# Kernel optimization log

Measured on AMD Instinct MI355X. Metric: run time of the kernel, lower is better.

The kernel has to match this reference:

```python
import jax, jax.numpy as jnp
import numpy as np
import math

B, L, H = 2, 2048, 2048
NH, HD, RD = 16, 128, 64
QR, KVR = 768, 512


def rotate_half(x):
    d = x.shape[-1]
    x1, x2 = x[..., : d // 2], x[..., d // 2 :]
    return jnp.concatenate([-x2, x1], axis=-1)


def apply_rope(x):
    # x: [B, L, H, D] or [B, L, D]
    d = x.shape[-1]
    seq_len = x.shape[1]
    inv_freq = 1.0 / (10000.0 ** (jnp.arange(0, d, 2, dtype=x.dtype) / d))
    pos = jnp.arange(seq_len, dtype=x.dtype)
    freqs = jnp.outer(pos, inv_freq)  # [L, d/2]
    cos = jnp.concatenate([jnp.cos(freqs), jnp.cos(freqs)], axis=-1)  # [L, d]
    sin = jnp.concatenate([jnp.sin(freqs), jnp.sin(freqs)], axis=-1)
    if x.ndim == 4:
        cos, sin = cos[None, :, None, :], sin[None, :, None, :]
    else:
        cos, sin = cos[None, :, :], sin[None, :, :]
    return x * cos + rotate_half(x) * sin


def setup_inputs() -> dict:
    key = jax.random.key(0)
    ks = jax.random.split(key, 9)
    sc = lambda fan_in: 1.0 / math.sqrt(fan_in)
    return {
        "x": jax.random.normal(ks[0], (B, L, H), jnp.float32),
        "wq_down": jax.random.normal(ks[1], (H, QR), jnp.float32) * sc(H),
        "wq_up": jax.random.normal(ks[2], (QR, NH * HD), jnp.float32) * sc(QR),
        "wq_rope": jax.random.normal(ks[3], (QR, NH * RD), jnp.float32) * sc(QR),
        "wkv_down": jax.random.normal(ks[4], (H, KVR), jnp.float32) * sc(H),
        "wk_up": jax.random.normal(ks[5], (KVR, NH * HD), jnp.float32) * sc(KVR),
        "wv_up": jax.random.normal(ks[6], (KVR, NH * HD), jnp.float32) * sc(KVR),
        "wk_rope": jax.random.normal(ks[7], (H, RD), jnp.float32) * sc(H),
        "wo": jax.random.normal(ks[8], (NH * HD, H), jnp.float32) * sc(NH * HD),
    }


def reference(x, wq_down, wq_up, wq_rope, wkv_down, wk_up, wv_up, wk_rope, wo):
    b, l, _ = x.shape
    # Q low-rank path
    q_latent = x @ wq_down                              # [B,L,QR]
    q_content = (q_latent @ wq_up).reshape(b, l, NH, HD)
    q_rope = (q_latent @ wq_rope).reshape(b, l, NH, RD)
    q_rope = apply_rope(q_rope)
    # KV joint low-rank path
    kv_latent = x @ wkv_down                            # [B,L,KVR]
    k_content = (kv_latent @ wk_up).reshape(b, l, NH, HD)
    v = (kv_latent @ wv_up).reshape(b, l, NH, HD)
    # decoupled RoPE key (shared across heads)
    k_rope = apply_rope(x @ wk_rope)                    # [B,L,RD]
    k_rope = jnp.broadcast_to(k_rope[:, :, None, :], (b, l, NH, RD))
    q = jnp.concatenate([q_content, q_rope], axis=-1)   # [B,L,NH,HD+RD]
    k = jnp.concatenate([k_content, k_rope], axis=-1)
    scale = 1.0 / math.sqrt(HD + RD)
    scores = jnp.einsum("bqhd,bkhd->bhqk", q, k) * scale
    causal_mask = jnp.triu(jnp.ones((l, l), dtype=bool), k=1)
    scores = jnp.where(causal_mask[None, None], -jnp.inf, scores)
    attn = jax.nn.softmax(scores, axis=-1)
    out = jnp.einsum("bhqk,bkhd->bqhd", attn, v).reshape(b, l, NH * HD)
    return out @ wo
```

## Files before the change

### kernel.cpp

```cpp
#include <hip/hip_runtime.h>

typedef unsigned short u16;
typedef unsigned int u32;
typedef unsigned long long u64;
typedef __bf16 bf16x8 __attribute__((ext_vector_type(8)));
typedef float f32x4 __attribute__((ext_vector_type(4)));
typedef float f32x16 __attribute__((ext_vector_type(16)));
typedef u32 u32x4 __attribute__((ext_vector_type(4)));

#define DEV static __device__ __forceinline__

constexpr int B_ = 2, L_ = 2048, H_ = 2048;
constexpr int NH_ = 16, HD_ = 128, RD_ = 64;
constexpr int QR_ = 768, KVR_ = 512;
constexpr int BL_ = B_ * L_;
constexpr int QKD_ = HD_ + RD_;
constexpr int QKS_ = NH_ * QKD_;
constexpr int NHHD_ = NH_ * HD_;
constexpr int ROWS_ = B_ * NH_ * L_;
constexpr float SCALE2 = 0.07216878364870322f * 1.4426950408889634f;

DEV u16 f2bf(float f) {
    __bf16 h = (__bf16)f;
    return __builtin_bit_cast(u16, h);
}
DEV float bf2f(u16 h) {
    u32 u = ((u32)h) << 16;
    return __builtin_bit_cast(float, u);
}
DEV u32 pk2(float lo, float hi) { return (u32)f2bf(lo) | ((u32)f2bf(hi) << 16); }
DEV bf16x8 ld8(const u16* p) { return __builtin_bit_cast(bf16x8, *(const u32x4*)p); }
DEV f32x4 mfma16(bf16x8 a, bf16x8 b, f32x4 c) {
    return __builtin_amdgcn_mfma_f32_16x16x32_bf16(a, b, c, 0, 0, 0);
}
DEV f32x16 mfma32(bf16x8 a, bf16x8 b, f32x16 c) {
    return __builtin_amdgcn_mfma_f32_32x32x16_bf16(a, b, c, 0, 0, 0);
}
DEV void gload16(const void* g, void* l) {
    __builtin_amdgcn_global_load_lds((const __attribute__((address_space(1))) void*)g,
                                     (__attribute__((address_space(3))) void*)l, 16, 0, 0);
}

__global__ __launch_bounds__(256) void cast_bf16_kernel(const float* __restrict__ src,
                                                        u16* __restrict__ dst, int n4) {
    int i = blockIdx.x * 256 + threadIdx.x;
    if (i >= n4) return;
    float4 v = ((const float4*)src)[i];
    u64 pk = (u64)f2bf(v.x) | ((u64)f2bf(v.y) << 16) | ((u64)f2bf(v.z) << 32) | ((u64)f2bf(v.w) << 48);
    ((u64*)dst)[i] = pk;
}

__global__ __launch_bounds__(256) void cast_transpose(const float* __restrict__ src, u16* __restrict__ dst,
                                                      int K, int N, int dstN) {
    __shared__ float tile[32][33];
    int n0 = blockIdx.x * 32, k0 = blockIdx.y * 32;
    int tx = threadIdx.x & 31, ty = threadIdx.x >> 5;
#pragma unroll
    for (int i = 0; i < 4; ++i) {
        int kk = ty + i * 8;
        int n = n0 + tx;
        tile[kk][tx] = (n < N) ? src[(size_t)(k0 + kk) * N + n] : 0.f;
    }
    __syncthreads();
#pragma unroll
    for (int i = 0; i < 4; ++i) {
        int nn = ty + i * 8;
        dst[(size_t)(n0 + nn) * K + k0 + tx] = f2bf(tile[tx][nn]);
    }
}

__global__ __launch_bounds__(256) void build_rope_tab(float2* __restrict__ tab) {
    int idx = blockIdx.x * 256 + threadIdx.x;
    int pos = idx >> 5, i = idx & 31;
    float freq = exp2f((float)i * (-13.287712379549449f / 32.f));
    float ang = (float)pos * freq;
    tab[idx] = make_float2(cosf(ang), sinf(ang));
}

template <int EPI>
__global__ __launch_bounds__(256, 2) void gemm_bt(const u16* __restrict__ A, int lda,
                                                  const u16* __restrict__ Bt,
                                                  void* __restrict__ Cv, void* __restrict__ Cv2,
                                                  int ldc, int K, const float2* __restrict__ tab) {
    __shared__ u16 As[128 * 64];
    __shared__ u16 Bs[128 * 64];
    const int tid = threadIdx.x;
    const int l = tid & 63, w = tid >> 6;
    const int l15 = l & 15, g = l >> 4;
    const int wr = w >> 1, wc = w & 1;
    const int bm = blockIdx.y * 128, bn = blockIdx.x * 128;

    const f32x4 zero = {0.f, 0.f, 0.f, 0.f};
    f32x4 acc[4][4];
#pragma unroll
    for (int m = 0; m < 4; ++m)
#pragma unroll
        for (int n = 0; n < 4; ++n) acc[m][n] = zero;

    int aoff[4], boff[4];
#pragma unroll
    for (int j = 0; j < 4; ++j) {
        int chunk = j * 256 + tid;
        int row = chunk >> 3, gr = chunk & 7;
        aoff[j] = row * lda + gr * 8;
        boff[j] = row * K + gr * 8;
    }
    const u16* Ab = A + (size_t)bm * lda;
    const u16* Bb = Bt + (size_t)bn * K;

    const int nK = K / 64;
    for (int kt = 0; kt < nK; ++kt) {
        const int ko = kt * 64;
        __syncthreads();
#pragma unroll
        for (int j = 0; j < 4; ++j) gload16(Ab + ko + aoff[j], As + j * 2048 + w * 512);
#pragma unroll
        for (int j = 0; j < 4; ++j) gload16(Bb + ko + boff[j], Bs + j * 2048 + w * 512);
        __syncthreads();
#pragma unroll
        for (int kk = 0; kk < 2; ++kk) {
            bf16x8 af[4], bfr[4];
#pragma unroll
            for (int m = 0; m < 4; ++m)
                af[m] = ld8(As + (wr * 64 + m * 16 + l15) * 64 + kk * 32 + g * 8);
#pragma unroll
            for (int n = 0; n < 4; ++n)
                bfr[n] = ld8(Bs + (wc * 64 + n * 16 + l15) * 64 + kk * 32 + g * 8);
#pragma unroll
            for (int m = 0; m < 4; ++m)
#pragma unroll
                for (int n = 0; n < 4; ++n) acc[m][n] = mfma16(af[m], bfr[n], acc[m][n]);
        }
    }

    if constexpr (EPI == 0 || EPI == 1) {
#pragma unroll
        for (int m = 0; m < 4; ++m)
#pragma unroll
            for (int n = 0; n < 4; ++n)
#pragma unroll
                for (int r = 0; r < 4; ++r) {
                    int row = bm + wr * 64 + m * 16 + g * 4 + r;
                    int col = bn + wc * 64 + n * 16 + l15;
                    if (EPI == 1)
                        ((float*)Cv)[(size_t)row * ldc + col] = acc[m][n][r];
                    else
                        ((u16*)Cv)[(size_t)row * ldc + col] = f2bf(acc[m][n][r]);
                }
    }
    if constexpr (EPI == 2) {
        const int base = bn + wc * 64;
        u16* qb = (u16*)Cv;
        if (base < 2048) {
            const int h = base >> 7, dbase = base & 127;
#pragma unroll
            for (int m = 0; m < 4; ++m)
#pragma unroll
                for (int n = 0; n < 4; ++n)
#pragma unroll
                    for (int r = 0; r < 4; ++r) {
                        int token = bm + wr * 64 + m * 16 + g * 4 + r;
                        qb[(size_t)token * QKS_ + h * QKD_ + dbase + n * 16 + l15] =
                            f2bf(acc[m][n][r] * SCALE2);
                    }
        } else {
            const int h = (base - 2048) >> 6;
#pragma unroll
            for (int m = 0; m < 4; ++m)
#pragma unroll
                for (int r = 0; r < 4; ++r) {
                    const int token = bm + wr * 64 + m * 16 + g * 4 + r;
                    const int pos = token & (L_ - 1);
                    u16* bp = qb + (size_t)token * QKS_ + h * QKD_ + HD_;
#pragma unroll
                    for (int n = 0; n < 2; ++n) {
                        const int i = n * 16 + l15;
                        float2 cs = tab[pos * 32 + i];
                        float x1 = acc[m][n][r], x2 = acc[m][n + 2][r];
                        bp[i] = f2bf((x1 * cs.x - x2 * cs.y) * SCALE2);
                        bp[i + 32] = f2bf((x2 * cs.x + x1 * cs.y) * SCALE2);
                    }
                }
        }
    }
    if constexpr (EPI == 3) {
        const int base = bn + wc * 64;
        if (base < 2048) {
            u16* kb = (u16*)Cv;
            const int h = base >> 7, dbase = base & 127;
#pragma unroll
            for (int m = 0; m < 4; ++m)
#pragma unroll
                for (int n = 0; n < 4; ++n)
#pragma unroll
                    for (int r = 0; r < 4; ++r) {
                        int token = bm + wr * 64 + m * 16 + g * 4 + r;
                        kb[(size_t)token * QKS_ + h * QKD_ + dbase + n * 16 + l15] =
                            f2bf(acc[m][n][r]);
                    }
        } else {
            u16* vtb = (u16*)Cv2;
            const int b = bm >> 11;
#pragma unroll
            for (int m = 0; m < 4; ++m)
#pragma unroll
                for (int n = 0; n < 4; ++n) {
                    const int vc = base - 2048 + n * 16 + l15;
                    const int qrow = (bm + wr * 64 + m * 16 + g * 4) & (L_ - 1);
                    u64 pk = (u64)pk2(acc[m][n][0], acc[m][n][1]) |
                             ((u64)pk2(acc[m][n][2], acc[m][n][3]) << 32);
                    *(u64*)(vtb + (size_t)(b * NHHD_ + vc) * L_ + qrow) = pk;
                }
        }
    }
}

__global__ __launch_bounds__(256) void rope_k_kernel(const u16* __restrict__ src, int S,
                                                     u16* __restrict__ dst,
                                                     const float2* __restrict__ tab) {
    int idx = blockIdx.x * 256 + threadIdx.x;
    int token = idx >> 5, i = idx & 31;
    int pos = token & (L_ - 1);
    float2 cs = tab[pos * 32 + i];
    float x1 = bf2f(src[(size_t)token * S + i]);
    float x2 = bf2f(src[(size_t)token * S + i + 32]);
    u16 o1 = f2bf(x1 * cs.x - x2 * cs.y);
    u16 o2 = f2bf(x2 * cs.x + x1 * cs.y);
    u16* base = dst + (size_t)token * QKS_ + HD_;
#pragma unroll
    for (int h = 0; h < NH_; ++h) {
        base[h * QKD_ + i] = o1;
        base[h * QKD_ + i + 32] = o2;
    }
}

__global__ __launch_bounds__(256, 2) void flash_attn(const u16* __restrict__ q, const u16* __restrict__ k,
                                                     const u16* __restrict__ vt,
                                                     float* __restrict__ opart, float* __restrict__ mlpart) {
    __shared__ __align__(16) u16 Ks[2][64 * 192];
    __shared__ __align__(16) u16 Vs[2][128 * 64];
    const int p = blockIdx.x >> 1, split = blockIdx.x & 1;
    const int h = blockIdx.y, b = blockIdx.z;
    const int tid = threadIdx.x, w = tid >> 6, l = tid & 63;
    const int ql = l & 31, hi = l >> 5;
    const int sw = ql & 7;

    const u16* kbase = k + (size_t)(b * L_) * QKS_ + h * QKD_;
    const u16* vtbase = vt + (size_t)(b * NHHD_ + h * HD_) * L_;

    int koff[6], voff[4];
#pragma unroll
    for (int j = 0; j < 6; ++j) {
        int off = j * 4096 + tid * 16;
        int row = off / 384;
        int gr = (off % 384) / 16;
        koff[j] = row * QKS_ + (gr ^ (row & 7)) * 8;
    }
#pragma unroll
    for (int j = 0; j < 4; ++j) {
        int off = j * 4096 + tid * 16;
        int row = off >> 7;
        int gr = (off >> 4) & 7;
        voff[j] = row * L_ + (gr ^ (row & 7)) * 8;
    }

    auto STAGE = [&](int buf, int kv0) {
        const u16* kb = kbase + (size_t)kv0 * QKS_;
#pragma unroll
        for (int j = 0; j < 6; ++j)
            gload16(kb + koff[j], (u16*)Ks[buf] + j * 2048 + w * 512);
        const u16* vb = vtbase + kv0;
#pragma unroll
        for (int j = 0; j < 4; ++j)
            gload16(vb + voff[j], (u16*)Vs[buf] + j * 2048 + w * 512);
    };

    for (int half = 0; half < 2; ++half) {
        const int qtile = half ? 15 - p : p;
        const int q0 = qtile * 128;
        const int qabs = q0 + w * 32 + ql;

        bf16x8 qf[12];
        {
            const u16* qrow = q + (size_t)(b * L_ + qabs) * QKS_ + h * QKD_;
#pragma unroll
            for (int c = 0; c < 12; ++c) qf[c] = ld8(qrow + c * 16 + hi * 8);
        }
        f32x16 o[4];
#pragma unroll
        for (int n = 0; n < 4; ++n)
#pragma unroll
            for (int r = 0; r < 16; ++r) o[n][r] = 0.f;
        float m2 = -1e30f, lsum = 0.f;

        const int nt = 2 * qtile + 2;
        __syncthreads();
        STAGE(0, split * 64);
        int i = 0;
        for (int t = split; t < nt; t += 2, ++i) {
            __syncthreads();
            if (t + 2 < nt) STAGE((i + 1) & 1, (t + 2) * 64);
            const u16* Kb = Ks[i & 1];
            const u16* Vb = Vs[i & 1];
            const int kv0 = t * 64;

            f32x16 s0, s1;
#pragma unroll
            for (int r = 0; r < 16; ++r) { s0[r] = 0.f; s1[r] = 0.f; }
#pragma unroll
            for (int c = 0; c < 12; ++c) {
                int gsw = ((2 * c + hi) ^ sw) * 16;
                bf16x8 k0 = ld8((const u16*)((const char*)Kb + ql * 384 + gsw));
                bf16x8 k1 = ld8((const u16*)((const char*)Kb + (32 + ql) * 384 + gsw));
                s0 = mfma32(k0, qf[c], s0);
                s1 = mfma32(k1, qf[c], s1);
            }

            const bool domask = (kv0 + 63 > q0);
            float mx = -3e38f;
#pragma unroll
            for (int r = 0; r < 16; ++r) {
                const int kk = (r & 3) + 8 * (r >> 2) + 4 * hi;
                float x0 = s0[r];
                float x1 = s1[r];
                if (domask) {
                    if (kv0 + kk > qabs) x0 = -3e38f;
                    if (kv0 + 32 + kk > qabs) x1 = -3e38f;
                }
                s0[r] = x0; s1[r] = x1;
                mx = fmaxf(mx, fmaxf(x0, x1));
            }
            mx = fmaxf(mx, __shfl_xor(mx, 32));
            const float mnew = fmaxf(m2, mx);
            const float f = exp2f(m2 - mnew);
            m2 = mnew;
            float sl = 0.f;
#pragma unroll
            for (int r = 0; r < 16; ++r) {
                float p0 = exp2f(s0[r] - m2);
                float p1 = exp2f(s1[r] - m2);
                s0[r] = p0; s1[r] = p1;
                sl += p0 + p1;
            }
            lsum = lsum * f + sl;
#pragma unroll
            for (int n = 0; n < 4; ++n)
#pragma unroll
                for (int r = 0; r < 16; ++r) o[n][r] *= f;

#pragma unroll
            for (int c = 0; c < 4; ++c) {
                const int rb = 8 * (c & 1);
                float p0, p1, p2, p3, p4, p5, p6, p7;
                if (c < 2) {
                    p0 = s0[rb + 0]; p1 = s0[rb + 1]; p2 = s0[rb + 2]; p3 = s0[rb + 3];
                    p4 = s0[rb + 4]; p5 = s0[rb + 5]; p6 = s0[rb + 6]; p7 = s0[rb + 7];
                } else {
                    p0 = s1[rb + 0]; p1 = s1[rb + 1]; p2 = s1[rb + 2]; p3 = s1[rb + 3];
                    p4 = s1[rb + 4]; p5 = s1[rb + 5]; p6 = s1[rb + 6]; p7 = s1[rb + 7];
                }
                u32 a0 = pk2(p0, p1), a1 = pk2(p2, p3);
                u32 b0 = pk2(p4, p5), b1 = pk2(p6, p7);
                u32 pa0 = (u32)__shfl_xor((int)a0, 32);
                u32 pa1 = (u32)__shfl_xor((int)a1, 32);
                u32 pb0 = (u32)__shfl_xor((int)b0, 32);
                u32 pb1 = (u32)__shfl_xor((int)b1, 32);
                u32x4 pw = {hi ? pb0 : a0, hi ? pb1 : a1, hi ? b0 : pa0, hi ? b1 : pa1};
                bf16x8 pf = __builtin_bit_cast(bf16x8, pw);
                const int gsw = ((2 * c + hi) ^ sw) * 16;
#pragma unroll
                for (int n = 0; n < 4; ++n) {
                    bf16x8 vf = ld8((const u16*)((const char*)Vb + (32 * n + ql) * 128 + gsw));
                    o[n] = mfma32(vf, pf, o[n]);
                }
            }
        }

        const float ltot = lsum + __shfl_xor(lsum, 32);
        const int row = ((b * NH_ + h) << 11) + qabs;
        float* ob = opart + ((size_t)split * ROWS_ + row) * 128;
#pragma unroll
        for (int n = 0; n < 4; ++n)
#pragma unroll
            for (int rg = 0; rg < 4; ++rg) {
                f32x4 v = {o[n][4 * rg + 0], o[n][4 * rg + 1], o[n][4 * rg + 2], o[n][4 * rg + 3]};
                *(f32x4*)(ob + 32 * n + 8 * rg + 4 * hi) = v;
            }
        if (!hi) {
            float2 ml = {m2, ltot};
            *(float2*)(mlpart + ((size_t)split * ROWS_ + row) * 2) = ml;
        }
    }
}

__global__ __launch_bounds__(256) void combine_attn(const float* __restrict__ opart,
                                                    const float* __restrict__ mlpart,
                                                    u16* __restrict__ attn_o) {
    int idx = blockIdx.x * 256 + threadIdx.x;
    int row = idx >> 5, dq = (idx & 31) * 4;
    float2 ml0 = *(const float2*)(mlpart + (size_t)row * 2);
    float2 ml1 = *(const float2*)(mlpart + ((size_t)ROWS_ + row) * 2);
    float m = fmaxf(ml0.x, ml1.x);
    float w0 = exp2f(ml0.x - m), w1 = exp2f(ml1.x - m);
    float inv = 1.f / (w0 * ml0.y + w1 * ml1.y);
    w0 *= inv; w1 *= inv;
    f32x4 a = *(const f32x4*)(opart + (size_t)row * 128 + dq);
    f32x4 c = *(const f32x4*)(opart + ((size_t)ROWS_ + row) * 128 + dq);
    int b = row >> 15, h = (row >> 11) & 15, qrow = row & 2047;
    u16* dst = attn_o + (size_t)(b * L_ + qrow) * NHHD_ + h * HD_ + dq;
    u64 pk = (u64)pk2(a[0] * w0 + c[0] * w1, a[1] * w0 + c[1] * w1) |
             ((u64)pk2(a[2] * w0 + c[2] * w1, a[3] * w0 + c[3] * w1) << 32);
    *(u64*)dst = pk;
}

extern "C" void kernel_launch(void* const* d_in, const int* in_sizes, int n_in,
                              void* d_out, int out_size, void* d_ws, size_t ws_size,
                              hipStream_t stream) {
    (void)in_sizes; (void)n_in; (void)out_size; (void)ws_size;
    const float* x = (const float*)d_in[0];
    const float* wq_down = (const float*)d_in[1];
    const float* wq_up = (const float*)d_in[2];
    const float* wq_rope = (const float*)d_in[3];
    const float* wkv_down = (const float*)d_in[4];
    const float* wk_up = (const float*)d_in[5];
    const float* wv_up = (const float*)d_in[6];
    const float* wk_rope = (const float*)d_in[7];
    const float* wo = (const float*)d_in[8];

    u16* W = (u16*)d_ws;
    size_t off = 0;
    auto alloc = [&](size_t e) { u16* p = W + off; off += (e + 127) & ~(size_t)127; return p; };

    u16* xb    = alloc((size_t)BL_ * H_);
    u16* Wdn   = alloc((size_t)1408 * H_);
    u16* Wupq  = alloc((size_t)3072 * QR_);
    u16* Wupkv = alloc((size_t)4096 * KVR_);
    u16* Wo_t  = alloc((size_t)H_ * NHHD_);
    u16* tabm  = alloc((size_t)L_ * 32 * 4);
    u16* C1    = alloc((size_t)BL_ * 1408);
    u16* pad_  = alloc((size_t)28311552);
    u16* qbuf  = alloc((size_t)BL_ * QKS_);
    u16* kbuf  = alloc((size_t)BL_ * QKS_);
    u16* vt    = alloc((size_t)BL_ * NHHD_);
    u16* attn_o = alloc((size_t)BL_ * NHHD_);
    (void)pad_;

    float2* tab = (float2*)tabm;
    float* opart  = (float*)C1;
    float* mlpart = opart + (size_t)2 * ROWS_ * 128;

    cast_bf16_kernel<<<(BL_ * H_ / 4 + 255) / 256, 256, 0, stream>>>(x, xb, BL_ * H_ / 4);
    cast_transpose<<<dim3(QR_ / 32, H_ / 32), 256, 0, stream>>>(wq_down, Wdn, H_, QR_, QR_);
    cast_transpose<<<dim3(KVR_ / 32, H_ / 32), 256, 0, stream>>>(wkv_down, Wdn + (size_t)768 * H_, H_, KVR_, KVR_);
    cast_transpose<<<dim3(128 / 32, H_ / 32), 256, 0, stream>>>(wk_rope, Wdn + (size_t)1280 * H_, H_, RD_, 128);
    cast_transpose<<<dim3(NHHD_ / 32, QR_ / 32), 256, 0, stream>>>(wq_up, Wupq, QR_, NHHD_, NHHD_);
    cast_transpose<<<dim3(1024 / 32, QR_ / 32), 256, 0, stream>>>(wq_rope, Wupq + (size_t)2048 * QR_, QR_, 1024, 1024);
    cast_transpose<<<dim3(NHHD_ / 32, KVR_ / 32), 256, 0, stream>>>(wk_up, Wupkv, KVR_, NHHD_, NHHD_);
    cast_transpose<<<dim3(NHHD_ / 32, KVR_ / 32), 256, 0, stream>>>(wv_up, Wupkv + (size_t)2048 * KVR_, KVR_, NHHD_, NHHD_);
    cast_transpose<<<dim3(NHHD_ / 32, H_ / 32), 256, 0, stream>>>(wo, Wo_t, NHHD_, H_, H_);
    build_rope_tab<<<L_ * 32 / 256, 256, 0, stream>>>(tab);

    gemm_bt<0><<<dim3(1408 / 128, BL_ / 128), 256, 0, stream>>>(xb, H_, Wdn, C1, nullptr, 1408, H_, nullptr);
    gemm_bt<2><<<dim3(3072 / 128, BL_ / 128), 256, 0, stream>>>(C1, 1408, Wupq, qbuf, nullptr, 0, QR_, tab);
    gemm_bt<3><<<dim3(4096 / 128, BL_ / 128), 256, 0, stream>>>(C1 + 768, 1408, Wupkv, kbuf, vt, 0, KVR_, nullptr);

    rope_k_kernel<<<BL_ * 32 / 256, 256, 0, stream>>>(C1 + 1280, 1408, kbuf, tab);

    flash_attn<<<dim3(16, NH_, B_), 256, 0, stream>>>(qbuf, kbuf, vt, opart, mlpart);
    combine_attn<<<ROWS_ * 32 / 256, 256, 0, stream>>>(opart, mlpart, attn_o);

    gemm_bt<1><<<dim3(H_ / 128, BL_ / 128), 256, 0, stream>>>(attn_o, NHHD_, Wo_t, d_out, nullptr, H_, NHHD_, nullptr);
}
```

Baseline: 311.7 us.

## Fuse weight cast-transposes into one launch and map attention heads to XCDs

Replaces the eight separate weight cast-transpose launches with a single kernel. Each block works out its source tensor, destination and tile position from a flat block index. Separately, flash_attn now remaps the flat block id so that all 16 blocks of a given (batch, head) land on the same XCD under round-robin dispatch. Those blocks then share K/V tiles in that XCD's L2 instead of fetching them across dies. The cost is a small branch chain per transpose block and a dependence on the hardware's round-robin block-to-XCD assignment.

```diff
diff --git a/kernel.cpp b/kernel.cpp
--- a/kernel.cpp
+++ b/kernel.cpp
@@ -50,10 +50,24 @@
     ((u64*)dst)[i] = pk;
 }
 
-__global__ __launch_bounds__(256) void cast_transpose(const float* __restrict__ src, u16* __restrict__ dst,
-                                                      int K, int N, int dstN) {
+__global__ __launch_bounds__(256) void transpose_all(
+    const float* __restrict__ s0, const float* __restrict__ s1, const float* __restrict__ s2,
+    const float* __restrict__ s3, const float* __restrict__ s4, const float* __restrict__ s5,
+    const float* __restrict__ s6, const float* __restrict__ s7,
+    u16* __restrict__ Wdn, u16* __restrict__ Wupq, u16* __restrict__ Wupkv, u16* __restrict__ Wo_t) {
+    int t = blockIdx.x;
+    const float* src; u16* dst; int K, N, nx;
+    if (t < 1536)       {            src = s0; dst = Wdn;                          K = 2048; N = 768;  nx = 24; }
+    else if (t < 2560)  { t -= 1536; src = s1; dst = Wdn + (size_t)768 * 2048;     K = 2048; N = 512;  nx = 16; }
+    else if (t < 2816)  { t -= 2560; src = s2; dst = Wdn + (size_t)1280 * 2048;    K = 2048; N = 64;   nx = 4;  }
+    else if (t < 4352)  { t -= 2816; src = s3; dst = Wupq;                         K = 768;  N = 2048; nx = 64; }
+    else if (t < 5120)  { t -= 4352; src = s4; dst = Wupq + (size_t)2048 * 768;    K = 768;  N = 1024; nx = 32; }
+    else if (t < 6144)  { t -= 5120; src = s5; dst = Wupkv;                        K = 512;  N = 2048; nx = 64; }
+    else if (t < 7168)  { t -= 6144; src = s6; dst = Wupkv + (size_t)2048 * 512;   K = 512;  N = 2048; nx = 64; }
+    else                { t -= 7168; src = s7; dst = Wo_t;                         K = 2048; N = 2048; nx = 64; }
+    const int n0 = (t % nx) * 32, k0 = (t / nx) * 32;
+
     __shared__ float tile[32][33];
-    int n0 = blockIdx.x * 32, k0 = blockIdx.y * 32;
     int tx = threadIdx.x & 31, ty = threadIdx.x >> 5;
 #pragma unroll
     for (int i = 0; i < 4; ++i) {
@@ -239,8 +253,12 @@
                                                      float* __restrict__ opart, float* __restrict__ mlpart) {
     __shared__ __align__(16) u16 Ks[2][64 * 192];
     __shared__ __align__(16) u16 Vs[2][128 * 64];
-    const int p = blockIdx.x >> 1, split = blockIdx.x & 1;
-    const int h = blockIdx.y, b = blockIdx.z;
+    const int fid = blockIdx.x + 16 * blockIdx.y + 256 * blockIdx.z;
+    const int xcd = fid & 7, slot = fid >> 3;
+    const int group = xcd * 4 + (slot >> 4);
+    const int member = slot & 15;
+    const int b = group >> 4, h = group & 15;
+    const int p = member >> 1, split = member & 1;
     const int tid = threadIdx.x, w = tid >> 6, l = tid & 63;
     const int ql = l & 31, hi = l >> 5;
     const int sw = ql & 7;
@@ -450,14 +468,8 @@
     float* mlpart = opart + (size_t)2 * ROWS_ * 128;
 
     cast_bf16_kernel<<<(BL_ * H_ / 4 + 255) / 256, 256, 0, stream>>>(x, xb, BL_ * H_ / 4);
-    cast_transpose<<<dim3(QR_ / 32, H_ / 32), 256, 0, stream>>>(wq_down, Wdn, H_, QR_, QR_);
-    cast_transpose<<<dim3(KVR_ / 32, H_ / 32), 256, 0, stream>>>(wkv_down, Wdn + (size_t)768 * H_, H_, KVR_, KVR_);
-    cast_transpose<<<dim3(128 / 32, H_ / 32), 256, 0, stream>>>(wk_rope, Wdn + (size_t)1280 * H_, H_, RD_, 128);
-    cast_transpose<<<dim3(NHHD_ / 32, QR_ / 32), 256, 0, stream>>>(wq_up, Wupq, QR_, NHHD_, NHHD_);
-    cast_transpose<<<dim3(1024 / 32, QR_ / 32), 256, 0, stream>>>(wq_rope, Wupq + (size_t)2048 * QR_, QR_, 1024, 1024);
-    cast_transpose<<<dim3(NHHD_ / 32, KVR_ / 32), 256, 0, stream>>>(wk_up, Wupkv, KVR_, NHHD_, NHHD_);
-    cast_transpose<<<dim3(NHHD_ / 32, KVR_ / 32), 256, 0, stream>>>(wv_up, Wupkv + (size_t)2048 * KVR_, KVR_, NHHD_, NHHD_);
-    cast_transpose<<<dim3(NHHD_ / 32, H_ / 32), 256, 0, stream>>>(wo, Wo_t, NHHD_, H_, H_);
+    transpose_all<<<11264, 256, 0, stream>>>(wq_down, wkv_down, wk_rope, wq_up, wq_rope,
+                                             wk_up, wv_up, wo, Wdn, Wupq, Wupkv, Wo_t);
     build_rope_tab<<<L_ * 32 / 256, 256, 0, stream>>>(tab);
 
     gemm_bt<0><<<dim3(1408 / 128, BL_ / 128), 256, 0, stream>>>(xb, H_, Wdn, C1, nullptr, 1408, H_, nullptr);
```

Measured after the change: 289.7 us. -7.1%, faster.
